# Performance work log

Measured on AMD Instinct MI355X. Metric: run time of the kernel, lower is better.

The kernel has to match this reference:

```python
import jax, jax.numpy as jnp
import numpy as np

# static module config (matches init_kwargs)
DIM = 128
HEADS = 8
DW, HW, WW = 5, 7, 7  # depth/height/width window


def _neighbor_indices(D, H, W):
    """Flat circular-neighborhood indices, shape (P, n) with P=D*H*W, n=DW*HW*WW."""
    od = np.arange(DW) - (DW - 1) // 2
    oh = np.arange(HW) - (HW - 1) // 2
    ow = np.arange(WW) - (WW - 1) // 2
    dd = (np.arange(D)[:, None] + od[None, :]) % D   # (D, DW)
    hh = (np.arange(H)[:, None] + oh[None, :]) % H   # (H, HW)
    ww = (np.arange(W)[:, None] + ow[None, :]) % W   # (W, WW)
    idx = (dd[:, None, None, :, None, None] * (H * W)
           + hh[None, :, None, None, :, None] * W
           + ww[None, None, :, None, None, :])        # (D,H,W,DW,HW,WW)
    return jnp.asarray(idx.reshape(D * H * W, DW * HW * WW), dtype=jnp.int32)


def setup_inputs() -> dict:
    key = jax.random.key(0)
    k1, k2, k3, k4, k5 = jax.random.split(key, 5)
    B, D, H, W, C = 1, 5, 24, 48, DIM
    w_scale = 1.0 / np.sqrt(C)  # keep attention logits in a sane range
    return {
        "x": jax.random.normal(k1, (B, D, H, W, C), dtype=jnp.float32),
        "qkv_w": jax.random.normal(k2, (3 * C, C), dtype=jnp.float32) * w_scale,
        "qkv_b": jax.random.normal(k3, (3 * C,), dtype=jnp.float32) * 0.01,
        "proj_w": jax.random.normal(k4, (C, C), dtype=jnp.float32) * w_scale,
        "proj_b": jax.random.normal(k5, (C,), dtype=jnp.float32) * 0.01,
    }


def reference(x, qkv_w, qkv_b, proj_w, proj_b):
    B, D, H, W, C = x.shape
    P = D * H * W
    n = DW * HW * WW
    hd = C // HEADS
    scale = hd ** -0.5
    idx = _neighbor_indices(D, H, W)                      # (P, n) int32, static

    xf = x.reshape(B, P, C)
    qkv = xf @ qkv_w.T + qkv_b                            # (B, P, 3C)
    q, k, v = jnp.split(qkv, 3, axis=-1)

    q = q.reshape(B, P, HEADS, hd)                        # center-pixel query
    k_g = k[:, idx].reshape(B, P, n, HEADS, hd)           # gathered circular neighborhood
    v_g = v[:, idx].reshape(B, P, n, HEADS, hd)

    scores = jnp.einsum('bphd,bpnhd->bhpn', q, k_g) * scale
    attn = jax.nn.softmax(scores, axis=-1)                # softmax over 245 neighbors
    out = jnp.einsum('bhpn,bpnhd->bphd', attn, v_g).reshape(B, P, C)
    out = out @ proj_w.T + proj_b
    return out.reshape(B, D, H, W, C)
```

## Files before the change

### kernel.cpp

```cpp
#include <hip/hip_runtime.h>
#include <hip/hip_bf16.h>
#include <cstddef>

#define DIMC   128
#define NHEADS 8
#define HDIM   16
#define DD     5
#define HH     24
#define WW_    48
#define NPOS   (DD * HH * WW_)
#define SCALE  0.25f

typedef short  bf16x8 __attribute__((ext_vector_type(8)));
typedef float  f32x4  __attribute__((ext_vector_type(4)));

__device__ __forceinline__ unsigned short f2bf(float f) {
    unsigned u = __float_as_uint(f);
    u = (u + 0x7FFFu + ((u >> 16) & 1u)) >> 16;
    return (unsigned short)u;
}
__device__ __forceinline__ float bf2f(unsigned short s) {
    return __uint_as_float(((unsigned)s) << 16);
}

__global__ __launch_bounds__(256) void prep_kernel(
    const float* __restrict__ x,
    const float* __restrict__ wq,
    const float* __restrict__ wp,
    unsigned short* __restrict__ Axq,
    unsigned short* __restrict__ Bxq,
    unsigned short* __restrict__ Bxp)
{
    const int i = blockIdx.x * 256 + threadIdx.x;
    const bool isA = (i < 184320);
    const float* src; unsigned short* dst; int rel;
    if (isA)             { src = x;  dst = Axq; rel = i; }
    else if (i < 196608) { src = wq; dst = Bxq; rel = i - 184320; }
    else                 { src = wp; dst = Bxp; rel = i - 196608; }
    const int row = rel >> 5;
    const int c4  = rel & 31;
    const float4 v = *(const float4*)(src + (size_t)row * 128 + c4 * 4);
    ushort4 hi, lo;
    hi.x = f2bf(v.x); hi.y = f2bf(v.y); hi.z = f2bf(v.z); hi.w = f2bf(v.w);
    lo.x = f2bf(v.x - bf2f(hi.x));
    lo.y = f2bf(v.y - bf2f(hi.y));
    lo.z = f2bf(v.z - bf2f(hi.z));
    lo.w = f2bf(v.w - bf2f(hi.w));
    unsigned short* p = dst + (size_t)row * 384 + c4 * 4;
    if (isA) {
        *(ushort4*)(p)       = hi;
        *(ushort4*)(p + 128) = lo;
        *(ushort4*)(p + 256) = hi;
    } else {
        *(ushort4*)(p)       = hi;
        *(ushort4*)(p + 128) = hi;
        *(ushort4*)(p + 256) = lo;
    }
}

template <int MI, int EPI>
__global__ __launch_bounds__(256, 3) void gemm_mfma_kernel(
    const unsigned short* __restrict__ Ax,
    const unsigned short* __restrict__ Bx,
    const float* __restrict__ bias,
    float* __restrict__ C, int ldc,
    float* __restrict__ Qf32,
    unsigned short* __restrict__ Kbf,
    unsigned short* __restrict__ Vbf)
{
    __shared__ __align__(16) unsigned short Bs[64][392];

    const int tid = threadIdx.x;
    const int bn  = blockIdx.x * 64;
    const int bm  = blockIdx.y * 64 * MI;

    for (int i = tid; i < 64 * 48; i += 256) {
        const int r = i / 48, s = i % 48;
        *(ulonglong2*)(&Bs[r][s * 8]) =
            *(const ulonglong2*)(Bx + (size_t)(bn + r) * 384 + s * 8);
    }
    __syncthreads();

    const int w    = tid >> 6;
    const int lane = tid & 63;
    const int ln   = lane & 15;
    const int quad = lane >> 4;

    f32x4 acc[MI][4] = {};
    const unsigned short* arow[MI];
    #pragma unroll
    for (int mi = 0; mi < MI; ++mi)
        arow[mi] = Ax + (size_t)(bm + w * 16 * MI + mi * 16 + ln) * 384 + quad * 8;

    #pragma unroll
    for (int kc = 0; kc < 12; ++kc) {
        bf16x8 a[MI];
        #pragma unroll
        for (int mi = 0; mi < MI; ++mi) a[mi] = *(const bf16x8*)(arow[mi] + kc * 32);
        #pragma unroll
        for (int nt = 0; nt < 4; ++nt) {
            const bf16x8 b = *(const bf16x8*)(&Bs[nt * 16 + ln][kc * 32 + quad * 8]);
            #pragma unroll
            for (int mi = 0; mi < MI; ++mi)
                acc[mi][nt] = __builtin_amdgcn_mfma_f32_16x16x32_bf16(a[mi], b, acc[mi][nt], 0, 0, 0);
        }
    }

    #pragma unroll
    for (int mi = 0; mi < MI; ++mi)
        #pragma unroll
        for (int nt = 0; nt < 4; ++nt) {
            const int col = bn + nt * 16 + ln;
            const float bv = bias[col];
            #pragma unroll
            for (int r = 0; r < 4; ++r) {
                const int row = bm + w * 16 * MI + mi * 16 + quad * 4 + r;
                const float val = acc[mi][nt][r] + bv;
                if (EPI == 0) {
                    C[(size_t)row * ldc + col] = val;
                } else {
                    if (col < 128) {
                        Qf32[(size_t)row * 128 + col] = val;
                    } else if (col < 256) {
                        Kbf[(size_t)row * 128 + (col - 128)] = f2bf(val);
                    } else {
                        Vbf[(size_t)row * 128 + (col - 256)] = f2bf(val);
                    }
                }
            }
        }
}

__global__ __launch_bounds__(320, 2) void attn_kernel(
    const float* __restrict__ Qf32,
    const unsigned short* __restrict__ Kbf,
    const unsigned short* __restrict__ Vbf,
    unsigned short* __restrict__ Ap)
{
    __shared__ __align__(16) unsigned short Vt[16][520];
    __shared__ __align__(16) unsigned short Qb[80][40];
    __shared__ __align__(16) unsigned short Pw[5][2][16][40];
    __shared__ unsigned short Mb2[16][34];
    __shared__ int RowL[512];

    const int tile = blockIdx.x;
    const int h    = blockIdx.y;
    const int ty0  = (tile / 12) * 4;
    const int tx0  = (tile % 12) * 4;
    const int tid  = threadIdx.x;

    for (int u = tid; u < 512; u += 320) {
        const int uc = u < 500 ? u : 499;
        const int dp = uc / 100, rr = uc % 100;
        const int uy = rr / 10,  ux = rr % 10;
        int y = ty0 - 3 + uy; if (y < 0) y += HH;  if (y >= HH) y -= HH;
        int x = tx0 - 3 + ux; if (x < 0) x += WW_; if (x >= WW_) x -= WW_;
        RowL[u] = (dp * HH + y) * WW_ + x;
    }
    for (int i = tid; i < 512; i += 320) {
        const int t = i >> 4, ln = i & 15;
        const int sy = ln >> 2, sx = ln & 3;
        unsigned bits = 0;
        #pragma unroll
        for (int b = 0; b < 16; ++b) {
            const int u = t * 16 + b;
            const int rr = u % 100;
            const int uy = rr / 10, ux = rr % 10;
            if (u < 500 && (unsigned)(uy - sy) <= 6u && (unsigned)(ux - sx) <= 6u)
                bits |= 1u << b;
        }
        Mb2[ln][t] = (unsigned short)bits;
    }
    for (int i = tid; i < 256; i += 320) {
        const int u0 = i * 2;
        unsigned short va[16], vb[16];
        #pragma unroll
        for (int c = 0; c < 16; ++c) { va[c] = 0; vb[c] = 0; }
        #pragma unroll
        for (int half = 0; half < 2; ++half) {
            const int u = u0 + half;
            if (u < 500) {
                const int dp = u / 100, rr = u % 100;
                const int uy = rr / 10,  ux = rr % 10;
                int y = ty0 - 3 + uy; if (y < 0) y += HH;  if (y >= HH) y -= HH;
                int x = tx0 - 3 + ux; if (x < 0) x += WW_; if (x >= WW_) x -= WW_;
                const int g = (dp * HH + y) * WW_ + x;
                const bf16x8 p0 = *(const bf16x8*)(Vbf + (size_t)g * 128 + h * 16);
                const bf16x8 p1 = *(const bf16x8*)(Vbf + (size_t)g * 128 + h * 16 + 8);
                unsigned short* dst = half ? vb : va;
                #pragma unroll
                for (int c = 0; c < 8; ++c) { dst[c] = (unsigned short)p0[c]; dst[8 + c] = (unsigned short)p1[c]; }
            }
        }
        #pragma unroll
        for (int c = 0; c < 16; ++c)
            *(unsigned*)(&Vt[c][u0]) = (unsigned)va[c] | ((unsigned)vb[c] << 16);
    }
    for (int i = tid; i < 1280; i += 320) {
        const int p = i >> 4, c = i & 15;
        const int d = p >> 4, s = p & 15;
        const int sy = s >> 2, sx = s & 3;
        const int g = (d * HH + ty0 + sy) * WW_ + tx0 + sx;
        const float qv = Qf32[(size_t)g * 128 + h * 16 + c];
        const unsigned short hi = f2bf(qv);
        Qb[p][c]      = hi;
        Qb[p][16 + c] = f2bf(qv - bf2f(hi));
    }
    __syncthreads();

    const int w    = tid >> 6;
    const int lane = tid & 63;
    const int ln   = lane & 15;
    const int quad = lane >> 4;

    const bf16x8 qf = *(const bf16x8*)(&Qb[w * 16 + ln][quad * 8]);
    f32x4 Ow = {0.f, 0.f, 0.f, 0.f};
    float lsum = 0.f;

    const float C1 = SCALE * 1.44269504f;
    const float C0 = -11.5415603f;

    const int koff = h * 16 + (quad & 1) * 8;
    bf16x8 k0 = *(const bf16x8*)(Kbf + (size_t)RowL[ln]      * 128 + koff);
    bf16x8 k1 = *(const bf16x8*)(Kbf + (size_t)RowL[16 + ln] * 128 + koff);

    #pragma unroll 2
    for (int c = 0; c < 16; ++c) {
        const int u0 = c * 32;
        bf16x8 n0 = k0, n1 = k1;
        if (c < 15) {
            const int g0 = RowL[u0 + 32 + ln];
            const int g1 = RowL[u0 + 48 + ln];
            n0 = *(const bf16x8*)(Kbf + (size_t)g0 * 128 + koff);
            n1 = *(const bf16x8*)(Kbf + (size_t)g1 * 128 + koff);
        }
        const unsigned mb = *(const unsigned*)(&Mb2[ln][2 * c]);
        const unsigned m0 = (mb >> (quad * 4)) & 0xF;
        const unsigned m1 = (mb >> (16 + quad * 4)) & 0xF;

        f32x4 s0 = __builtin_amdgcn_mfma_f32_16x16x32_bf16(k0, qf, (f32x4){0.f,0.f,0.f,0.f}, 0, 0, 0);
        f32x4 s1 = __builtin_amdgcn_mfma_f32_16x16x32_bf16(k1, qf, (f32x4){0.f,0.f,0.f,0.f}, 0, 0, 0);

        unsigned short* pw = &Pw[w][c & 1][ln][0];
        #pragma unroll
        for (int t = 0; t < 2; ++t) {
            const f32x4 s = t ? s1 : s0;
            const unsigned m = t ? m1 : m0;
            unsigned eu[4];
            #pragma unroll
            for (int r = 0; r < 4; ++r) {
                const float arg = ((m >> r) & 1u) ? fmaf(s[r], C1, C0) : -100.f;
                const unsigned trunc = __float_as_uint(exp2f(arg)) & 0xFFFF0000u;
                eu[r] = trunc;
                lsum += __uint_as_float(trunc);
            }
            unsigned* dst = (unsigned*)(pw + t * 16 + quad * 4);
            dst[0] = (eu[0] >> 16) | eu[1];
            dst[1] = (eu[2] >> 16) | eu[3];
        }

        const bf16x8 vf = *(const bf16x8*)(&Vt[ln][u0 + quad * 8]);
        const bf16x8 pf = *(const bf16x8*)(&Pw[w][c & 1][ln][quad * 8]);
        Ow = __builtin_amdgcn_mfma_f32_16x16x32_bf16(vf, pf, Ow, 0, 0, 0);

        k0 = n0; k1 = n1;
    }

    lsum += __shfl_xor(lsum, 16);
    lsum += __shfl_xor(lsum, 32);
    const float inv = 1.0f / lsum;

    const int sy = ln >> 2, sx = ln & 3;
    const size_t g = (size_t)((w * HH + ty0 + sy) * WW_ + (tx0 + sx));
    ushort4 hi4, lo4;
    {
        float v0 = Ow[0] * inv, v1 = Ow[1] * inv, v2 = Ow[2] * inv, v3 = Ow[3] * inv;
        hi4.x = f2bf(v0); lo4.x = f2bf(v0 - bf2f(hi4.x));
        hi4.y = f2bf(v1); lo4.y = f2bf(v1 - bf2f(hi4.y));
        hi4.z = f2bf(v2); lo4.z = f2bf(v2 - bf2f(hi4.z));
        hi4.w = f2bf(v3); lo4.w = f2bf(v3 - bf2f(hi4.w));
    }
    unsigned short* row = Ap + g * 384 + h * HDIM + quad * 4;
    *(ushort4*)(row)       = hi4;
    *(ushort4*)(row + 128) = lo4;
    *(ushort4*)(row + 256) = hi4;
}

extern "C" void kernel_launch(void* const* d_in, const int* in_sizes, int n_in,
                              void* d_out, int out_size, void* d_ws, size_t ws_size,
                              hipStream_t stream)
{
    const float* x      = (const float*)d_in[0];
    const float* qkv_w  = (const float*)d_in[1];
    const float* qkv_b  = (const float*)d_in[2];
    const float* proj_w = (const float*)d_in[3];
    const float* proj_b = (const float*)d_in[4];
    float* out = (float*)d_out;

    char* ws = (char*)d_ws;
    unsigned short* Axq = (unsigned short*)ws;  ws += (size_t)NPOS * 384 * 2;
    unsigned short* Ap  = (unsigned short*)ws;  ws += (size_t)NPOS * 384 * 2;
    unsigned short* Bxq = (unsigned short*)ws;  ws += (size_t)384 * 384 * 2;
    unsigned short* Bxp = (unsigned short*)ws;  ws += (size_t)128 * 384 * 2;
    float*          Qf  = (float*)ws;           ws += (size_t)NPOS * 128 * 4;
    unsigned short* Kbf = (unsigned short*)ws;  ws += (size_t)NPOS * 128 * 2;
    unsigned short* Vbf = (unsigned short*)ws;  ws += (size_t)NPOS * 128 * 2;

    prep_kernel<<<784, 256, 0, stream>>>(x, qkv_w, proj_w, Axq, Bxq, Bxp);

    {
        dim3 grid(384 / 64, NPOS / 64);
        gemm_mfma_kernel<1, 1><<<grid, 256, 0, stream>>>(
            Axq, Bxq, qkv_b, nullptr, 0, Qf, Kbf, Vbf);
    }
    {
        dim3 grid(72, NHEADS);
        attn_kernel<<<grid, 320, 0, stream>>>(Qf, Kbf, Vbf, Ap);
    }
    {
        dim3 grid(DIMC / 64, NPOS / 64);
        gemm_mfma_kernel<1, 0><<<grid, 256, 0, stream>>>(
            Ap, Bxp, proj_b, out, DIMC, nullptr, nullptr, nullptr);
    }
}
```

Baseline: 109.0 us.

## Split attention neighbor chunks across two wave groups and stream GEMM B from global

```diff
diff --git a/kernel.cpp b/kernel.cpp
--- a/kernel.cpp
+++ b/kernel.cpp
@@ -58,8 +58,8 @@
     }
 }
 
-template <int MI, int EPI>
-__global__ __launch_bounds__(256, 3) void gemm_mfma_kernel(
+template <int EPI>
+__global__ __launch_bounds__(256, 4) void gemm_stream_kernel(
     const unsigned short* __restrict__ Ax,
     const unsigned short* __restrict__ Bx,
     const float* __restrict__ bias,
@@ -68,70 +68,58 @@
     unsigned short* __restrict__ Kbf,
     unsigned short* __restrict__ Vbf)
 {
-    __shared__ __align__(16) unsigned short Bs[64][392];
-
-    const int tid = threadIdx.x;
-    const int bn  = blockIdx.x * 64;
-    const int bm  = blockIdx.y * 64 * MI;
-
-    for (int i = tid; i < 64 * 48; i += 256) {
-        const int r = i / 48, s = i % 48;
-        *(ulonglong2*)(&Bs[r][s * 8]) =
-            *(const ulonglong2*)(Bx + (size_t)(bn + r) * 384 + s * 8);
-    }
-    __syncthreads();
-
+    const int tid  = threadIdx.x;
     const int w    = tid >> 6;
     const int lane = tid & 63;
     const int ln   = lane & 15;
     const int quad = lane >> 4;
-
-    f32x4 acc[MI][4] = {};
-    const unsigned short* arow[MI];
-    #pragma unroll
-    for (int mi = 0; mi < MI; ++mi)
-        arow[mi] = Ax + (size_t)(bm + w * 16 * MI + mi * 16 + ln) * 384 + quad * 8;
-
+    const int bn   = blockIdx.x * 64;
+    const int bm   = blockIdx.y * 64;
+
+    const unsigned short* aptr = Ax + (size_t)(bm + w * 16 + ln) * 384 + quad * 8;
+    const unsigned short* bptr0 = Bx + (size_t)(bn + ln) * 384 + quad * 8;
+    const unsigned short* bptr1 = bptr0 + (size_t)16 * 384;
+    const unsigned short* bptr2 = bptr0 + (size_t)32 * 384;
+    const unsigned short* bptr3 = bptr0 + (size_t)48 * 384;
+
+    f32x4 acc[4] = {};
     #pragma unroll
     for (int kc = 0; kc < 12; ++kc) {
-        bf16x8 a[MI];
-        #pragma unroll
-        for (int mi = 0; mi < MI; ++mi) a[mi] = *(const bf16x8*)(arow[mi] + kc * 32);
-        #pragma unroll
-        for (int nt = 0; nt < 4; ++nt) {
-            const bf16x8 b = *(const bf16x8*)(&Bs[nt * 16 + ln][kc * 32 + quad * 8]);
-            #pragma unroll
-            for (int mi = 0; mi < MI; ++mi)
-                acc[mi][nt] = __builtin_amdgcn_mfma_f32_16x16x32_bf16(a[mi], b, acc[mi][nt], 0, 0, 0);
-        }
+        const bf16x8 a  = *(const bf16x8*)(aptr  + kc * 32);
+        const bf16x8 b0 = *(const bf16x8*)(bptr0 + kc * 32);
+        const bf16x8 b1 = *(const bf16x8*)(bptr1 + kc * 32);
+        const bf16x8 b2 = *(const bf16x8*)(bptr2 + kc * 32);
+        const bf16x8 b3 = *(const bf16x8*)(bptr3 + kc * 32);
+        acc[0] = __builtin_amdgcn_mfma_f32_16x16x32_bf16(a, b0, acc[0], 0, 0, 0);
+        acc[1] = __builtin_amdgcn_mfma_f32_16x16x32_bf16(a, b1, acc[1], 0, 0, 0);
+        acc[2] = __builtin_amdgcn_mfma_f32_16x16x32_bf16(a, b2, acc[2], 0, 0, 0);
+        acc[3] = __builtin_amdgcn_mfma_f32_16x16x32_bf16(a, b3, acc[3], 0, 0, 0);
     }
 
     #pragma unroll
-    for (int mi = 0; mi < MI; ++mi)
-        #pragma unroll
-        for (int nt = 0; nt < 4; ++nt) {
-            const int col = bn + nt * 16 + ln;
-            const float bv = bias[col];
-            #pragma unroll
-            for (int r = 0; r < 4; ++r) {
-                const int row = bm + w * 16 * MI + mi * 16 + quad * 4 + r;
-                const float val = acc[mi][nt][r] + bv;
-                if (EPI == 0) {
-                    C[(size_t)row * ldc + col] = val;
+    for (int nt = 0; nt < 4; ++nt) {
+        const int col = bn + nt * 16 + ln;
+        const float bv = bias[col];
+        #pragma unroll
+        for (int r = 0; r < 4; ++r) {
+            const int row = bm + w * 16 + quad * 4 + r;
+            const float val = acc[nt][r] + bv;
+            if (EPI == 0) {
+                C[(size_t)row * ldc + col] = val;
+            } else {
+                if (col < 128) {
+                    Qf32[(size_t)row * 128 + col] = val;
+                } else if (col < 256) {
+                    Kbf[(size_t)row * 128 + (col - 128)] = f2bf(val);
                 } else {
-                    if (col < 128) {
-                        Qf32[(size_t)row * 128 + col] = val;
-                    } else if (col < 256) {
-                        Kbf[(size_t)row * 128 + (col - 128)] = f2bf(val);
-                    } else {
-                        Vbf[(size_t)row * 128 + (col - 256)] = f2bf(val);
-                    }
+                    Vbf[(size_t)row * 128 + (col - 256)] = f2bf(val);
                 }
             }
         }
-}
-
-__global__ __launch_bounds__(320, 2) void attn_kernel(
+    }
+}
+
+__global__ __launch_bounds__(640, 5) void attn_kernel(
     const float* __restrict__ Qf32,
     const unsigned short* __restrict__ Kbf,
     const unsigned short* __restrict__ Vbf,
@@ -139,9 +127,11 @@
 {
     __shared__ __align__(16) unsigned short Vt[16][520];
     __shared__ __align__(16) unsigned short Qb[80][40];
-    __shared__ __align__(16) unsigned short Pw[5][2][16][40];
+    __shared__ __align__(16) unsigned short Pw[10][2][16][40];
     __shared__ unsigned short Mb2[16][34];
     __shared__ int RowL[512];
+    float* redO  = (float*)&Vt[0][0];
+    __shared__ float red_l[10][16];
 
     const int tile = blockIdx.x;
     const int h    = blockIdx.y;
@@ -149,7 +139,7 @@
     const int tx0  = (tile % 12) * 4;
     const int tid  = threadIdx.x;
 
-    for (int u = tid; u < 512; u += 320) {
+    for (int u = tid; u < 512; u += 640) {
         const int uc = u < 500 ? u : 499;
         const int dp = uc / 100, rr = uc % 100;
         const int uy = rr / 10,  ux = rr % 10;
@@ -157,9 +147,9 @@
         int x = tx0 - 3 + ux; if (x < 0) x += WW_; if (x >= WW_) x -= WW_;
         RowL[u] = (dp * HH + y) * WW_ + x;
     }
-    for (int i = tid; i < 512; i += 320) {
-        const int t = i >> 4, ln = i & 15;
-        const int sy = ln >> 2, sx = ln & 3;
+    for (int i = tid; i < 512; i += 640) {
+        const int t = i >> 4, ql = i & 15;
+        const int sy = ql >> 2, sx = ql & 3;
         unsigned bits = 0;
         #pragma unroll
         for (int b = 0; b < 16; ++b) {
@@ -169,9 +159,9 @@
             if (u < 500 && (unsigned)(uy - sy) <= 6u && (unsigned)(ux - sx) <= 6u)
                 bits |= 1u << b;
         }
-        Mb2[ln][t] = (unsigned short)bits;
-    }
-    for (int i = tid; i < 256; i += 320) {
+        Mb2[ql][t] = (unsigned short)bits;
+    }
+    for (int i = tid; i < 256; i += 640) {
         const int u0 = i * 2;
         unsigned short va[16], vb[16];
         #pragma unroll
@@ -196,7 +186,7 @@
         for (int c = 0; c < 16; ++c)
             *(unsigned*)(&Vt[c][u0]) = (unsigned)va[c] | ((unsigned)vb[c] << 16);
     }
-    for (int i = tid; i < 1280; i += 320) {
+    for (int i = tid; i < 1280; i += 640) {
         const int p = i >> 4, c = i & 15;
         const int d = p >> 4, s = p & 15;
         const int sy = s >> 2, sx = s & 3;
@@ -208,12 +198,14 @@
     }
     __syncthreads();
 
-    const int w    = tid >> 6;
-    const int lane = tid & 63;
-    const int ln   = lane & 15;
-    const int quad = lane >> 4;
-
-    const bf16x8 qf = *(const bf16x8*)(&Qb[w * 16 + ln][quad * 8]);
+    const int w     = tid >> 6;
+    const int wslab = w % 5;
+    const int c0    = (w / 5) * 8;
+    const int lane  = tid & 63;
+    const int ln    = lane & 15;
+    const int quad  = lane >> 4;
+
+    const bf16x8 qf = *(const bf16x8*)(&Qb[wslab * 16 + ln][quad * 8]);
     f32x4 Ow = {0.f, 0.f, 0.f, 0.f};
     float lsum = 0.f;
 
@@ -221,18 +213,16 @@
     const float C0 = -11.5415603f;
 
     const int koff = h * 16 + (quad & 1) * 8;
-    bf16x8 k0 = *(const bf16x8*)(Kbf + (size_t)RowL[ln]      * 128 + koff);
-    bf16x8 k1 = *(const bf16x8*)(Kbf + (size_t)RowL[16 + ln] * 128 + koff);
+    bf16x8 k0 = *(const bf16x8*)(Kbf + (size_t)RowL[c0 * 32 + ln]      * 128 + koff);
+    bf16x8 k1 = *(const bf16x8*)(Kbf + (size_t)RowL[c0 * 32 + 16 + ln] * 128 + koff);
 
     #pragma unroll 2
-    for (int c = 0; c < 16; ++c) {
+    for (int c = c0; c < c0 + 8; ++c) {
         const int u0 = c * 32;
         bf16x8 n0 = k0, n1 = k1;
-        if (c < 15) {
-            const int g0 = RowL[u0 + 32 + ln];
-            const int g1 = RowL[u0 + 48 + ln];
-            n0 = *(const bf16x8*)(Kbf + (size_t)g0 * 128 + koff);
-            n1 = *(const bf16x8*)(Kbf + (size_t)g1 * 128 + koff);
+        if (c < c0 + 7) {
+            n0 = *(const bf16x8*)(Kbf + (size_t)RowL[u0 + 32 + ln] * 128 + koff);
+            n1 = *(const bf16x8*)(Kbf + (size_t)RowL[u0 + 48 + ln] * 128 + koff);
         }
         const unsigned mb = *(const unsigned*)(&Mb2[ln][2 * c]);
         const unsigned m0 = (mb >> (quad * 4)) & 0xF;
@@ -268,22 +258,39 @@
 
     lsum += __shfl_xor(lsum, 16);
     lsum += __shfl_xor(lsum, 32);
-    const float inv = 1.0f / lsum;
-
-    const int sy = ln >> 2, sx = ln & 3;
-    const size_t g = (size_t)((w * HH + ty0 + sy) * WW_ + (tx0 + sx));
-    ushort4 hi4, lo4;
-    {
-        float v0 = Ow[0] * inv, v1 = Ow[1] * inv, v2 = Ow[2] * inv, v3 = Ow[3] * inv;
-        hi4.x = f2bf(v0); lo4.x = f2bf(v0 - bf2f(hi4.x));
-        hi4.y = f2bf(v1); lo4.y = f2bf(v1 - bf2f(hi4.y));
-        hi4.z = f2bf(v2); lo4.z = f2bf(v2 - bf2f(hi4.z));
-        hi4.w = f2bf(v3); lo4.w = f2bf(v3 - bf2f(hi4.w));
-    }
-    unsigned short* row = Ap + g * 384 + h * HDIM + quad * 4;
-    *(ushort4*)(row)       = hi4;
-    *(ushort4*)(row + 128) = lo4;
-    *(ushort4*)(row + 256) = hi4;
+
+    __syncthreads();
+
+    if (quad == 0) red_l[w][ln] = lsum;
+    #pragma unroll
+    for (int r = 0; r < 4; ++r)
+        redO[(size_t)(w * 16 + quad * 4 + r) * 16 + ln] = Ow[r];
+    __syncthreads();
+
+    if (tid < 320) {
+        const float l = red_l[w][ln] + red_l[w + 5][ln];
+        const float inv = 1.0f / l;
+        f32x4 o;
+        #pragma unroll
+        for (int r = 0; r < 4; ++r)
+            o[r] = redO[(size_t)(w * 16 + quad * 4 + r) * 16 + ln]
+                 + redO[(size_t)((w + 5) * 16 + quad * 4 + r) * 16 + ln];
+
+        const int sy = ln >> 2, sx = ln & 3;
+        const size_t g = (size_t)((w * HH + ty0 + sy) * WW_ + (tx0 + sx));
+        ushort4 hi4, lo4;
+        {
+            float v0 = o[0] * inv, v1 = o[1] * inv, v2 = o[2] * inv, v3 = o[3] * inv;
+            hi4.x = f2bf(v0); lo4.x = f2bf(v0 - bf2f(hi4.x));
+            hi4.y = f2bf(v1); lo4.y = f2bf(v1 - bf2f(hi4.y));
+            hi4.z = f2bf(v2); lo4.z = f2bf(v2 - bf2f(hi4.z));
+            hi4.w = f2bf(v3); lo4.w = f2bf(v3 - bf2f(hi4.w));
+        }
+        unsigned short* row = Ap + g * 384 + h * HDIM + quad * 4;
+        *(ushort4*)(row)       = hi4;
+        *(ushort4*)(row + 128) = lo4;
+        *(ushort4*)(row + 256) = hi4;
+    }
 }
 
 extern "C" void kernel_launch(void* const* d_in, const int* in_sizes, int n_in,
@@ -310,16 +317,16 @@
 
     {
         dim3 grid(384 / 64, NPOS / 64);
-        gemm_mfma_kernel<1, 1><<<grid, 256, 0, stream>>>(
+        gemm_stream_kernel<1><<<grid, 256, 0, stream>>>(
             Axq, Bxq, qkv_b, nullptr, 0, Qf, Kbf, Vbf);
     }
     {
         dim3 grid(72, NHEADS);
-        attn_kernel<<<grid, 320, 0, stream>>>(Qf, Kbf, Vbf, Ap);
+        attn_kernel<<<grid, 640, 0, stream>>>(Qf, Kbf, Vbf, Ap);
     }
     {
         dim3 grid(DIMC / 64, NPOS / 64);
-        gemm_mfma_kernel<1, 0><<<grid, 256, 0, stream>>>(
+        gemm_stream_kernel<0><<<grid, 256, 0, stream>>>(
             Ap, Bxp, proj_b, out, DIMC, nullptr, nullptr, nullptr);
     }
 }
```

Measured after the change: 124.2 us. 14.0% more time.
